# Performance work log

Measured on AMD Instinct MI355X. Metric: run time of the kernel, lower is better.

Reference implementation:

```python
import jax, jax.numpy as jnp
import numpy as np

NEG = -1e30  # safe -inf surrogate for log-space DP
BLANK = 0    # torch.nn.CTCLoss default blank index


def _ctc_loss_sum(lp, labels, in_lens, lab_lens):
    """CTC negative log-likelihood, summed over batch.
    lp: [T, B, V] log-probabilities; labels: [B, L] int; in_lens, lab_lens: [B] int.
    """
    T, B, V = lp.shape
    L = labels.shape[1]
    S = 2 * L + 1  # extended label length (blanks interleaved)
    s = jnp.arange(S)
    # extended label sequence z: blank at even positions, label at odd
    ext = jnp.where(s % 2 == 0, BLANK, labels[:, jnp.clip((s - 1) // 2, 0, L - 1)])  # [B,S]
    ext_m2 = jnp.concatenate([jnp.full((B, 2), BLANK, ext.dtype), ext[:, :-2]], axis=1)
    skip = (s >= 2) & (ext != BLANK) & (ext != ext_m2)  # [B,S] skip-transition allowed
    # emission log-probs gathered at extended labels: [T,B,S]
    emit = jnp.take_along_axis(lp, jnp.broadcast_to(ext[None], (T, B, S)), axis=2)
    alpha0 = jnp.full((B, S), NEG, lp.dtype)
    alpha0 = alpha0.at[:, 0].set(emit[0, :, 0]).at[:, 1].set(emit[0, :, 1])

    def step(alpha, inputs):
        emit_t, t = inputs
        a1 = jnp.concatenate([jnp.full((B, 1), NEG, alpha.dtype), alpha[:, :-1]], axis=1)
        a2 = jnp.concatenate([jnp.full((B, 2), NEG, alpha.dtype), alpha[:, :-2]], axis=1)
        comb = jnp.logaddexp(alpha, a1)
        comb = jnp.where(skip, jnp.logaddexp(comb, a2), comb)
        new = comb + emit_t
        # past each sequence's length, freeze alpha
        new = jnp.where(t < in_lens[:, None], new, alpha)
        return new, None

    alpha, _ = jax.lax.scan(step, alpha0, (emit[1:], jnp.arange(1, T)))
    s_last = 2 * lab_lens  # final blank position per sample
    bidx = jnp.arange(B)
    ll = jnp.logaddexp(alpha[bidx, s_last], alpha[bidx, s_last - 1])
    return jnp.sum(-ll)


def setup_inputs() -> dict:
    key = jax.random.key(0)
    k1, k2, k3, k4, k5, k6 = jax.random.split(key, 6)
    B, T, H, V, L = 16, 512, 512, 4096, 64
    hs_pad = jax.random.normal(k1, (B, T, H), dtype=jnp.float32)
    hs_lens = jax.random.randint(k2, (B,), T // 2, T + 1, dtype=jnp.int32)
    ys_pad = jax.random.randint(k3, (B, L), 1, V, dtype=jnp.int32)  # avoid blank=0
    ys_lens = jax.random.randint(k4, (B,), L // 2, L + 1, dtype=jnp.int32)
    W = jax.random.normal(k5, (H, V), dtype=jnp.float32) * (H ** -0.5)
    b = jax.random.normal(k6, (V,), dtype=jnp.float32) * 0.01
    return {"hs_pad": hs_pad, "hs_lens": hs_lens, "ys_pad": ys_pad,
            "ys_lens": ys_lens, "W": W, "b": b}


def reference(hs_pad, hs_lens, ys_pad, ys_lens, W, b):
    # projection (dropout_rate=0.0 -> identity) + log_softmax
    logits = jnp.einsum('bth,hv->btv', hs_pad, W) + b
    log_probs = jax.nn.log_softmax(logits, axis=-1)
    lp = jnp.transpose(log_probs, (1, 0, 2))  # [T,B,V]
    B = lp.shape[1]
    loss = _ctc_loss_sum(lp, ys_pad, hs_lens, ys_lens)
    return loss / B
```

## Files before the change

### kernel.cpp

```cpp
#include <hip/hip_runtime.h>
#include <hip/hip_bf16.h>
#include <math.h>

#define BB   16
#define TT   512
#define HH   512
#define VV   4096
#define LL   64
#define SS   129
#define JJ   65
#define MM   (BB*TT)

#define LOG2E 1.4426950408889634f
#define LN2   0.6931471805599453f

typedef __bf16 bf16;
typedef __attribute__((ext_vector_type(4))) __bf16 bf16x4;
typedef __attribute__((ext_vector_type(8))) __bf16 bf16x8;
typedef __attribute__((ext_vector_type(4))) float f32x4;

template<int CTRL>
__device__ __forceinline__ float dpp_mov(float x) {
    return __int_as_float(__builtin_amdgcn_update_dpp(
        __float_as_int(x), __float_as_int(x), CTRL, 0xF, 0xF, false));
}
__device__ __forceinline__ float row16_max(float x) {
    x = fmaxf(x, dpp_mov<0x128>(x));
    x = fmaxf(x, dpp_mov<0x124>(x));
    x = fmaxf(x, dpp_mov<0x122>(x));
    x = fmaxf(x, dpp_mov<0x121>(x));
    return x;
}
__device__ __forceinline__ float row16_sum(float x) {
    x += dpp_mov<0x128>(x);
    x += dpp_mov<0x124>(x);
    x += dpp_mov<0x122>(x);
    x += dpp_mov<0x121>(x);
    return x;
}
__device__ __forceinline__ float dpp_shr1_zero(float x) {
    int r = __builtin_amdgcn_update_dpp(0, __float_as_int(x),
                                        0x138 , 0xF, 0xF, false);
    return __int_as_float(r);
}
template<int CTRL>
__device__ __forceinline__ float dpp_max_t(float m) {
    int r = __builtin_amdgcn_update_dpp(0, __float_as_int(m), CTRL, 0xF, 0xF, false);
    return fmaxf(m, __int_as_float(r));
}

__global__ __launch_bounds__(256) void prep(const float* __restrict__ hs,
                                            const float* __restrict__ W,
                                            bf16* __restrict__ Abf,
                                            bf16* __restrict__ Wt,
                                            float* __restrict__ out)
{
    __shared__ float t[64][65];
    const int tid = threadIdx.x;
    int bx = blockIdx.x;
    if (bx == 0 && tid == 0) out[0] = 0.f;
    if (bx < 4096) {
        int idx = bx * 256 + tid;
        float4 v = ((const float4*)hs)[idx];
        bf16x4 o = {(bf16)v.x, (bf16)v.y, (bf16)v.z, (bf16)v.w};
        *(bf16x4*)(Abf + (size_t)idx * 4) = o;
    } else {
        bx -= 4096;
        const int n0 = (bx & 63) * 64;
        const int k0 = (bx >> 6) * 64;
        #pragma unroll
        for (int i = 0; i < 16; ++i) {
            int idx = tid + i * 256;
            int kk = idx >> 6, nn = idx & 63;
            t[kk][nn] = W[(size_t)(k0 + kk) * VV + n0 + nn];
        }
        __syncthreads();
        #pragma unroll
        for (int i = 0; i < 16; ++i) {
            int idx = tid + i * 256;
            int nl = idx >> 6, kk = idx & 63;
            Wt[(size_t)(n0 + nl) * HH + k0 + kk] = (bf16)t[kk][nl];
        }
    }
}

#define TN 128
#define NT64 (VV / 64)

#define GLDS(src, dst) \
    __builtin_amdgcn_global_load_lds((const __attribute__((address_space(1))) void*)(src), \
                                     (__attribute__((address_space(3))) void*)(dst), 16, 0, 0)

__global__ __launch_bounds__(256) void gemm_lse_mfma(
    const bf16* __restrict__ A,
    const bf16* __restrict__ Bt,
    const float* __restrict__ bias,
    const int*  __restrict__ ys,
    float* __restrict__ part,
    float* __restrict__ glpT)
{
    __shared__ bf16 As[128 * 32];
    __shared__ bf16 Bs[128 * 32];
    const int tid = threadIdx.x;
    const int lane = tid & 63;
    const int wid = tid >> 6;
    const int wm = wid >> 1, wn = wid & 1;
    const int m0 = blockIdx.y * 128, n0 = blockIdx.x * 128;
    const int lq = lane & 15, kg = lane >> 4;

    f32x4 acc[4][4];
    const f32x4 z = {0.f, 0.f, 0.f, 0.f};
    #pragma unroll
    for (int i = 0; i < 4; ++i)
        #pragma unroll
        for (int j = 0; j < 4; ++j) acc[i][j] = z;

    const int c0 = tid;
    const int row0 = c0 >> 2, sl0 = (c0 & 3) ^ ((row0 >> 1) & 3);
    const int c1 = tid + 256;
    const int row1 = c1 >> 2, sl1 = (c1 & 3) ^ ((row1 >> 1) & 3);
    bf16* dstA0 = As + (size_t)(0 * 256 + (tid & 192)) * 8;
    bf16* dstA1 = As + (size_t)(1 * 256 + (tid & 192)) * 8;
    bf16* dstB0 = Bs + (size_t)(0 * 256 + (tid & 192)) * 8;
    bf16* dstB1 = Bs + (size_t)(1 * 256 + (tid & 192)) * 8;
    const bf16* srcA0 = A  + (size_t)(m0 + row0) * HH + sl0 * 8;
    const bf16* srcA1 = A  + (size_t)(m0 + row1) * HH + sl1 * 8;
    const bf16* srcB0 = Bt + (size_t)(n0 + row0) * HH + sl0 * 8;
    const bf16* srcB1 = Bt + (size_t)(n0 + row1) * HH + sl1 * 8;

    for (int k0 = 0; k0 < HH; k0 += 32) {
        GLDS(srcA0 + k0, dstA0);
        GLDS(srcA1 + k0, dstA1);
        GLDS(srcB0 + k0, dstB0);
        GLDS(srcB1 + k0, dstB1);
        __syncthreads();
        bf16x8 a[4], b[4];
        #pragma unroll
        for (int i = 0; i < 4; ++i) {
            int ar = wm * 64 + i * 16 + lq;
            a[i] = *(const bf16x8*)&As[ar * 32 + ((kg ^ ((ar >> 1) & 3)) * 8)];
        }
        #pragma unroll
        for (int j = 0; j < 4; ++j) {
            int br = wn * 64 + j * 16 + lq;
            b[j] = *(const bf16x8*)&Bs[br * 32 + ((kg ^ ((br >> 1) & 3)) * 8)];
        }
        #pragma unroll
        for (int i = 0; i < 4; ++i)
            #pragma unroll
            for (int j = 0; j < 4; ++j)
                acc[i][j] = __builtin_amdgcn_mfma_f32_16x16x32_bf16(a[i], b[j], acc[i][j], 0, 0, 0);
        __syncthreads();
    }

    const int ct = blockIdx.x * 2 + wn;
    float bj[4];
    #pragma unroll
    for (int j = 0; j < 4; ++j) bj[j] = bias[n0 + wn * 64 + j * 16 + lq];
    #pragma unroll
    for (int i = 0; i < 4; ++i) {
        #pragma unroll
        for (int r = 0; r < 4; ++r) {
            float v[4], mx = -3.4e38f;
            #pragma unroll
            for (int j = 0; j < 4; ++j) { v[j] = acc[i][j][r] + bj[j]; mx = fmaxf(mx, v[j]); }
            mx = row16_max(mx);
            float sm = 0.f;
            #pragma unroll
            for (int j = 0; j < 4; ++j) sm += __expf(v[j] - mx);
            sm = row16_sum(sm);
            if (lq == 0) {
                int rowg = m0 + wm * 64 + i * 16 + kg * 4 + r;
                size_t o = ((size_t)rowg * NT64 + ct) * 2;
                part[o] = mx; part[o + 1] = sm;
            }
        }
    }

    const int bidx = m0 >> 9;
    const int t0s  = (m0 & 511) + wm * 64;
    const int nbase = n0 + wn * 64;
    for (int j = 0; j < JJ; ++j) {
        int c = (j == 0) ? 0 : ys[bidx * LL + j - 1];
        int local = c - nbase;
        if (local >= 0 && local < 64) {
            int cl = local & 15;
            float bc = bias[c];
            #pragma unroll
            for (int jt = 0; jt < 4; ++jt) {
                if ((local >> 4) == jt && lq == cl) {
                    #pragma unroll
                    for (int i = 0; i < 4; ++i)
                        #pragma unroll
                        for (int r = 0; r < 4; ++r) {
                            int tt = t0s + i * 16 + kg * 4 + r;
                            glpT[(size_t)(bidx * JJ + j) * TT + tt] = acc[i][jt][r] + bc;
                        }
                }
            }
        }
    }
}

#define LOADN(pA0,pA1,pA2,pA3,qA0,qA1,qA2,qA3, blk) { \
    int bb_ = (blk); bb_ = bb_ < 32 ? bb_ : 31; \
    const float4* p0_ = (const float4*)(g0 + bb_ * 16); \
    const float4* pB_ = (const float4*)(gB + bb_ * 16); \
    pA0 = p0_[0]; pA1 = p0_[1]; pA2 = p0_[2]; pA3 = p0_[3]; \
    qA0 = pB_[0]; qA1 = pB_[1]; qA2 = pB_[2]; qA3 = pB_[3]; }

#define RV4(rv, base, p4, q4) \
    rv[base+0] = __builtin_amdgcn_exp2f((q4.x - p4.x) * LOG2E); \
    rv[base+1] = __builtin_amdgcn_exp2f((q4.y - p4.y) * LOG2E); \
    rv[base+2] = __builtin_amdgcn_exp2f((q4.z - p4.z) * LOG2E); \
    rv[base+3] = __builtin_amdgcn_exp2f((q4.w - p4.w) * LOG2E);

#define CSUM(p4) (((p4).x + (p4).y) + ((p4).z + (p4).w))
#define CMSK(p4, tb) \
    ( (((tb)+0 >= 1) && ((tb)+0 < Tin) ? (p4).x : 0.f) \
    + (((tb)+1 >= 1) && ((tb)+1 < Tin) ? (p4).y : 0.f) \
    + (((tb)+2 >= 1) && ((tb)+2 < Tin) ? (p4).z : 0.f) \
    + (((tb)+3 >= 1) && ((tb)+3 < Tin) ? (p4).w : 0.f) )

#define RVCN(rv, pA0,pA1,pA2,pA3,qA0,qA1,qA2,qA3, blk) { \
    const int tB_ = (blk) * 16; \
    RV4(rv, 0,  pA0, qA0); RV4(rv, 4,  pA1, qA1); \
    RV4(rv, 8,  pA2, qA2); RV4(rv, 12, pA3, qA3); \
    if (tB_ > 0 && tB_ + 16 <= Tin) { \
        corr += (CSUM(pA0) + CSUM(pA1)) + (CSUM(pA2) + CSUM(pA3)); \
    } else { \
        corr += (CMSK(pA0, tB_) + CMSK(pA1, tB_ + 4)) \
              + (CMSK(pA2, tB_ + 8) + CMSK(pA3, tB_ + 12)); \
    } }

#define RESCALE() { \
        float m_ = fmaxf(fmaxf(vA ? A : 0.f, vB ? B : 0.f), vC ? C : 0.f); \
        m_ = dpp_max_t<0x111>(m_);  \
        m_ = dpp_max_t<0x112>(m_);  \
        m_ = dpp_max_t<0x114>(m_);  \
        m_ = dpp_max_t<0x118>(m_);  \
        m_ = dpp_max_t<0x142>(m_);  \
        m_ = dpp_max_t<0x143>(m_);  \
        int mb = __builtin_amdgcn_readlane(__float_as_int(m_), 63); \
        int k_ = ((mb >> 23) & 0xFF) - 127; \
        float sc = __int_as_float((127 - k_) << 23); \
        A *= sc; B *= sc; C *= sc; K += k_; \
    }

#define DO16N(rv, blk) { \
    const int tB_ = (blk) * 16; \
    if (tB_ > 0 && tB_ + 16 <= Tin) { \
        _Pragma("unroll") \
        for (int u = 0; u < 16; ++u) { \
            float prevB = dpp_shr1_zero(B); \
            float nA = A + prevB; \
            float t1 = A + B; \
            float t2 = skipB ? prevB : 0.f; \
            float nB = (t1 + t2) * rv[u]; \
            float nC = C + B; \
            A = nA; B = nB; C = nC; \
            if (u == 7 || u == 15) RESCALE(); \
        } \
    } else { \
        _Pragma("unroll") \
        for (int u = 0; u < 16; ++u) { \
            int t_ = tB_ + u; \
            bool upd = (t_ >= 1) && (t_ < Tin); \
            float prevB = dpp_shr1_zero(B); \
            float nA = A + prevB; \
            float t1 = A + B; \
            float t2 = skipB ? prevB : 0.f; \
            float nB = (t1 + t2) * rv[u]; \
            float nC = C + B; \
            A = upd ? nA : A; B = upd ? nB : B; C = upd ? nC : C; \
            if (u == 7 || u == 15) RESCALE(); \
        } \
    } }

__global__ __launch_bounds__(256) void ctc_tail(
    const float* __restrict__ glpT, const float* __restrict__ part,
    const int* __restrict__ ys, const int* __restrict__ hs_lens,
    const int* __restrict__ ys_lens, float* __restrict__ out)
{
    __shared__ float lsum_sh[4];
    const int b = blockIdx.x;
    const int tid = threadIdx.x;
    const int wave = tid >> 6;
    const int lane = tid & 63;
    const int Tin = hs_lens[b];
    const int Ll  = ys_lens[b];

    float v1 = 0.f, v2 = 0.f, corr = 0.f;
    int K = 0;

    if (wave == 0) {
        const int l = lane;
        const float* g0 = glpT + (size_t)(b * JJ) * TT;
        const float* gB = glpT + (size_t)(b * JJ + l + 1) * TT;

        const bool vA = (l <= Ll);
        const bool vB = (l <  Ll);
        const bool vC = (l == 63) && (Ll == 64);

        int cc = ys[b * LL + l];
        bool skipB = false;
        if (l >= 1) { int cp = ys[b * LL + l - 1]; skipB = (cc != 0) && (cc != cp); }

        float raw0_0 = g0[0];
        float d0 = (gB[0] - raw0_0) * LOG2E;
        float A = (l == 0) ? 1.0f : 0.0f;
        float B = (l == 0) ? __builtin_amdgcn_exp2f(d0) : 0.0f;
        float C = 0.0f;
        corr = raw0_0;

        float4 pa0, pa1, pa2, pa3, qa0, qa1, qa2, qa3;
        float4 pb0, pb1, pb2, pb3, qb0, qb1, qb2, qb3;
        float rva[16], rvb[16];
        LOADN(pa0,pa1,pa2,pa3,qa0,qa1,qa2,qa3, 0);
        LOADN(pb0,pb1,pb2,pb3,qb0,qb1,qb2,qb3, 1);
        for (int blk = 0; blk < 32; blk += 2) {
            RVCN(rva, pa0,pa1,pa2,pa3,qa0,qa1,qa2,qa3, blk);
            LOADN(pa0,pa1,pa2,pa3,qa0,qa1,qa2,qa3, blk + 2);
            DO16N(rva, blk);
            RVCN(rvb, pb0,pb1,pb2,pb3,qb0,qb1,qb2,qb3, blk + 1);
            LOADN(pb0,pb1,pb2,pb3,qb0,qb1,qb2,qb3, blk + 3);
            DO16N(rvb, blk + 1);
            if (16 * (blk + 2) >= Tin) break;
        }

        v1 = (Ll == 64) ? __shfl(C, 63, 64) : __shfl(A, Ll, 64);
        v2 = __shfl(B, Ll - 1, 64);
    } else {
        const int t0 = (wave - 1) * 171;
        const int t1 = (t0 + 171 < TT) ? (t0 + 171) : TT;
        const int grp = lane >> 4, li = lane & 15;
        float lsum = 0.f;
        for (int t = t0 + grp; t < t1; t += 4) {
            const float* p = part + ((size_t)(b * TT + t)) * (NT64 * 2) + li * 8;
            float4 a  = ((const float4*)p)[0];
            float4 c4 = ((const float4*)p)[1];
            float ml = fmaxf(fmaxf(a.x, a.z), fmaxf(c4.x, c4.z));
            float sl = a.y  * __expf(a.x  - ml) + a.w  * __expf(a.z  - ml)
                     + c4.y * __expf(c4.x - ml) + c4.w * __expf(c4.z - ml);
            float wm = row16_max(ml);
            float ss = row16_sum(sl * __expf(ml - wm));
            if (li == 0 && t < Tin) lsum += wm + logf(ss);
        }
        #pragma unroll
        for (int d = 1; d < 64; d <<= 1) lsum += __shfl_xor(lsum, d);
        if (lane == 0) lsum_sh[wave] = lsum;
    }
    __syncthreads();
    if (tid == 0) {
        float lsumT = lsum_sh[1] + lsum_sh[2] + lsum_sh[3];
        float ll2 = __builtin_amdgcn_logf(v1 + v2) + (float)K + (corr - lsumT) * LOG2E;
        atomicAdd(out, (-ll2 * LN2) * (1.0f / (float)BB));
    }
}

extern "C" void kernel_launch(void* const* d_in, const int* in_sizes, int n_in,
                              void* d_out, int out_size, void* d_ws, size_t ws_size,
                              hipStream_t stream) {
    const float* hs      = (const float*)d_in[0];
    const int*   hs_lens = (const int*)  d_in[1];
    const int*   ys      = (const int*)  d_in[2];
    const int*   ys_lens = (const int*)  d_in[3];
    const float* W       = (const float*)d_in[4];
    const float* bias    = (const float*)d_in[5];
    float* out = (float*)d_out;

    float* ws   = (float*)d_ws;
    float* part = ws;
    float* glpT = part + (size_t)MM * NT64 * 2;
    bf16*  Abf  = (bf16*)(glpT + (size_t)BB * JJ * TT);
    bf16*  Wt   = Abf + (size_t)MM * HH;

    prep<<<4608, 256, 0, stream>>>(hs, W, Abf, Wt, out);
    gemm_lse_mfma<<<dim3(VV / TN, MM / 128), 256, 0, stream>>>(Abf, Wt, bias, ys, part, glpT);
    ctc_tail<<<BB, 256, 0, stream>>>(glpT, part, ys, hs_lens, ys_lens, out);
}
```

Before: 179.9 us.

## Double GEMM K-tile to 64 and interleave CTC emission exp with recurrence

The GEMM+LSE kernel now stages K=64 per iteration, with an 8-slot XOR swizzle for LDS and two MFMA sub-steps per barrier pair. This halves the number of __syncthreads and global-to-LDS rounds, at the cost of doubling LDS use per block. The CTC recurrence no longer precomputes 16-entry ratio arrays and no longer has a separate unmasked fast path. Instead, exp values are computed per 4-step group and used immediately with masked updates, which lowers register pressure but adds mask selects on every step.

```diff
diff --git a/kernel.cpp b/kernel.cpp
--- a/kernel.cpp
+++ b/kernel.cpp
@@ -99,8 +99,8 @@
     float* __restrict__ part,
     float* __restrict__ glpT)
 {
-    __shared__ bf16 As[128 * 32];
-    __shared__ bf16 Bs[128 * 32];
+    __shared__ bf16 As[128 * 64];
+    __shared__ bf16 Bs[128 * 64];
     const int tid = threadIdx.x;
     const int lane = tid & 63;
     const int wid = tid >> 6;
@@ -115,41 +115,44 @@
         #pragma unroll
         for (int j = 0; j < 4; ++j) acc[i][j] = z;
 
-    const int c0 = tid;
-    const int row0 = c0 >> 2, sl0 = (c0 & 3) ^ ((row0 >> 1) & 3);
-    const int c1 = tid + 256;
-    const int row1 = c1 >> 2, sl1 = (c1 & 3) ^ ((row1 >> 1) & 3);
-    bf16* dstA0 = As + (size_t)(0 * 256 + (tid & 192)) * 8;
-    bf16* dstA1 = As + (size_t)(1 * 256 + (tid & 192)) * 8;
-    bf16* dstB0 = Bs + (size_t)(0 * 256 + (tid & 192)) * 8;
-    bf16* dstB1 = Bs + (size_t)(1 * 256 + (tid & 192)) * 8;
-    const bf16* srcA0 = A  + (size_t)(m0 + row0) * HH + sl0 * 8;
-    const bf16* srcA1 = A  + (size_t)(m0 + row1) * HH + sl1 * 8;
-    const bf16* srcB0 = Bt + (size_t)(n0 + row0) * HH + sl0 * 8;
-    const bf16* srcB1 = Bt + (size_t)(n0 + row1) * HH + sl1 * 8;
-
-    for (int k0 = 0; k0 < HH; k0 += 32) {
-        GLDS(srcA0 + k0, dstA0);
-        GLDS(srcA1 + k0, dstA1);
-        GLDS(srcB0 + k0, dstB0);
-        GLDS(srcB1 + k0, dstB1);
+    const bf16* srcA[4];
+    const bf16* srcB[4];
+    #pragma unroll
+    for (int i = 0; i < 4; ++i) {
+        int c = tid + i * 256;
+        int row = c >> 3;
+        int slot = (c & 7) ^ (row & 7);
+        srcA[i] = A  + (size_t)(m0 + row) * HH + slot * 8;
+        srcB[i] = Bt + (size_t)(n0 + row) * HH + slot * 8;
+    }
+
+    for (int k0 = 0; k0 < HH; k0 += 64) {
+        #pragma unroll
+        for (int i = 0; i < 4; ++i)
+            GLDS(srcA[i] + k0, As + (size_t)(i * 256 + (tid & 192)) * 8);
+        #pragma unroll
+        for (int i = 0; i < 4; ++i)
+            GLDS(srcB[i] + k0, Bs + (size_t)(i * 256 + (tid & 192)) * 8);
         __syncthreads();
-        bf16x8 a[4], b[4];
-        #pragma unroll
-        for (int i = 0; i < 4; ++i) {
-            int ar = wm * 64 + i * 16 + lq;
-            a[i] = *(const bf16x8*)&As[ar * 32 + ((kg ^ ((ar >> 1) & 3)) * 8)];
-        }
-        #pragma unroll
-        for (int j = 0; j < 4; ++j) {
-            int br = wn * 64 + j * 16 + lq;
-            b[j] = *(const bf16x8*)&Bs[br * 32 + ((kg ^ ((br >> 1) & 3)) * 8)];
-        }
-        #pragma unroll
-        for (int i = 0; i < 4; ++i)
-            #pragma unroll
-            for (int j = 0; j < 4; ++j)
-                acc[i][j] = __builtin_amdgcn_mfma_f32_16x16x32_bf16(a[i], b[j], acc[i][j], 0, 0, 0);
+        #pragma unroll
+        for (int kk = 0; kk < 2; ++kk) {
+            bf16x8 a[4], b[4];
+            #pragma unroll
+            for (int i = 0; i < 4; ++i) {
+                int ar = wm * 64 + i * 16 + lq;
+                a[i] = *(const bf16x8*)&As[ar * 64 + (((kg + kk * 4) ^ (ar & 7)) * 8)];
+            }
+            #pragma unroll
+            for (int j = 0; j < 4; ++j) {
+                int br = wn * 64 + j * 16 + lq;
+                b[j] = *(const bf16x8*)&Bs[br * 64 + (((kg + kk * 4) ^ (br & 7)) * 8)];
+            }
+            #pragma unroll
+            for (int i = 0; i < 4; ++i)
+                #pragma unroll
+                for (int j = 0; j < 4; ++j)
+                    acc[i][j] = __builtin_amdgcn_mfma_f32_16x16x32_bf16(a[i], b[j], acc[i][j], 0, 0, 0);
+        }
         __syncthreads();
     }
 
@@ -208,30 +211,6 @@
     const float4* pB_ = (const float4*)(gB + bb_ * 16); \
     pA0 = p0_[0]; pA1 = p0_[1]; pA2 = p0_[2]; pA3 = p0_[3]; \
     qA0 = pB_[0]; qA1 = pB_[1]; qA2 = pB_[2]; qA3 = pB_[3]; }
-
-#define RV4(rv, base, p4, q4) \
-    rv[base+0] = __builtin_amdgcn_exp2f((q4.x - p4.x) * LOG2E); \
-    rv[base+1] = __builtin_amdgcn_exp2f((q4.y - p4.y) * LOG2E); \
-    rv[base+2] = __builtin_amdgcn_exp2f((q4.z - p4.z) * LOG2E); \
-    rv[base+3] = __builtin_amdgcn_exp2f((q4.w - p4.w) * LOG2E);
-
-#define CSUM(p4) (((p4).x + (p4).y) + ((p4).z + (p4).w))
-#define CMSK(p4, tb) \
-    ( (((tb)+0 >= 1) && ((tb)+0 < Tin) ? (p4).x : 0.f) \
-    + (((tb)+1 >= 1) && ((tb)+1 < Tin) ? (p4).y : 0.f) \
-    + (((tb)+2 >= 1) && ((tb)+2 < Tin) ? (p4).z : 0.f) \
-    + (((tb)+3 >= 1) && ((tb)+3 < Tin) ? (p4).w : 0.f) )
-
-#define RVCN(rv, pA0,pA1,pA2,pA3,qA0,qA1,qA2,qA3, blk) { \
-    const int tB_ = (blk) * 16; \
-    RV4(rv, 0,  pA0, qA0); RV4(rv, 4,  pA1, qA1); \
-    RV4(rv, 8,  pA2, qA2); RV4(rv, 12, pA3, qA3); \
-    if (tB_ > 0 && tB_ + 16 <= Tin) { \
-        corr += (CSUM(pA0) + CSUM(pA1)) + (CSUM(pA2) + CSUM(pA3)); \
-    } else { \
-        corr += (CMSK(pA0, tB_) + CMSK(pA1, tB_ + 4)) \
-              + (CMSK(pA2, tB_ + 8) + CMSK(pA3, tB_ + 12)); \
-    } }
 
 #define RESCALE() { \
         float m_ = fmaxf(fmaxf(vA ? A : 0.f, vB ? B : 0.f), vC ? C : 0.f); \
@@ -247,35 +226,32 @@
         A *= sc; B *= sc; C *= sc; K += k_; \
     }
 
-#define DO16N(rv, blk) { \
-    const int tB_ = (blk) * 16; \
-    if (tB_ > 0 && tB_ + 16 <= Tin) { \
-        _Pragma("unroll") \
-        for (int u = 0; u < 16; ++u) { \
-            float prevB = dpp_shr1_zero(B); \
-            float nA = A + prevB; \
-            float t1 = A + B; \
-            float t2 = skipB ? prevB : 0.f; \
-            float nB = (t1 + t2) * rv[u]; \
-            float nC = C + B; \
-            A = nA; B = nB; C = nC; \
-            if (u == 7 || u == 15) RESCALE(); \
-        } \
-    } else { \
-        _Pragma("unroll") \
-        for (int u = 0; u < 16; ++u) { \
-            int t_ = tB_ + u; \
-            bool upd = (t_ >= 1) && (t_ < Tin); \
-            float prevB = dpp_shr1_zero(B); \
-            float nA = A + prevB; \
-            float t1 = A + B; \
-            float t2 = skipB ? prevB : 0.f; \
-            float nB = (t1 + t2) * rv[u]; \
-            float nC = C + B; \
-            A = upd ? nA : A; B = upd ? nB : B; C = upd ? nC : C; \
-            if (u == 7 || u == 15) RESCALE(); \
-        } \
-    } }
+#define STEP1(rv, t_) { \
+        bool upd = ((t_) >= 1) && ((t_) < Tin); \
+        float prevB = dpp_shr1_zero(B); \
+        float nA = A + prevB; \
+        float t1 = A + B; \
+        float t2 = skipB ? prevB : 0.f; \
+        float nB = (t1 + t2) * (rv); \
+        float nC = C + B; \
+        A = upd ? nA : A; B = upd ? nB : B; C = upd ? nC : C; }
+
+#define DO4Q(p4, q4, tb) { \
+        float r0_ = __builtin_amdgcn_exp2f((q4.x - p4.x) * LOG2E); \
+        float r1_ = __builtin_amdgcn_exp2f((q4.y - p4.y) * LOG2E); \
+        float r2_ = __builtin_amdgcn_exp2f((q4.z - p4.z) * LOG2E); \
+        float r3_ = __builtin_amdgcn_exp2f((q4.w - p4.w) * LOG2E); \
+        corr += ((((tb)+0 >= 1) && ((tb)+0 < Tin)) ? p4.x : 0.f) \
+              + ((((tb)+1 >= 1) && ((tb)+1 < Tin)) ? p4.y : 0.f) \
+              + ((((tb)+2 >= 1) && ((tb)+2 < Tin)) ? p4.z : 0.f) \
+              + ((((tb)+3 >= 1) && ((tb)+3 < Tin)) ? p4.w : 0.f); \
+        STEP1(r0_, (tb)+0); STEP1(r1_, (tb)+1); \
+        STEP1(r2_, (tb)+2); STEP1(r3_, (tb)+3); }
+
+#define DOCHUNK16(P0,P1,P2,P3,Q0,Q1,Q2,Q3, blk) { \
+        const int tB_ = (blk) * 16; \
+        DO4Q(P0, Q0, tB_ + 0); DO4Q(P1, Q1, tB_ + 4);  RESCALE(); \
+        DO4Q(P2, Q2, tB_ + 8); DO4Q(P3, Q3, tB_ + 12); RESCALE(); }
 
 __global__ __launch_bounds__(256) void ctc_tail(
     const float* __restrict__ glpT, const float* __restrict__ part,
@@ -315,16 +291,13 @@
 
         float4 pa0, pa1, pa2, pa3, qa0, qa1, qa2, qa3;
         float4 pb0, pb1, pb2, pb3, qb0, qb1, qb2, qb3;
-        float rva[16], rvb[16];
         LOADN(pa0,pa1,pa2,pa3,qa0,qa1,qa2,qa3, 0);
         LOADN(pb0,pb1,pb2,pb3,qb0,qb1,qb2,qb3, 1);
         for (int blk = 0; blk < 32; blk += 2) {
-            RVCN(rva, pa0,pa1,pa2,pa3,qa0,qa1,qa2,qa3, blk);
+            DOCHUNK16(pa0,pa1,pa2,pa3,qa0,qa1,qa2,qa3, blk);
             LOADN(pa0,pa1,pa2,pa3,qa0,qa1,qa2,qa3, blk + 2);
-            DO16N(rva, blk);
-            RVCN(rvb, pb0,pb1,pb2,pb3,qb0,qb1,qb2,qb3, blk + 1);
+            DOCHUNK16(pb0,pb1,pb2,pb3,qb0,qb1,qb2,qb3, blk + 1);
             LOADN(pb0,pb1,pb2,pb3,qb0,qb1,qb2,qb3, blk + 3);
-            DO16N(rvb, blk + 1);
             if (16 * (blk + 2) >= Tin) break;
         }
 
```

Result: slower. 194.9 us (+8.3%).
